# Optimization experiments

Measured on AMD Instinct MI355X. Metric: run time of the kernel, lower is better.

The kernel has to match this reference:

```python
import jax, jax.numpy as jnp
import numpy as np

HIDDEN = 2048
HEADS = 16
HEAD_DIM = HIDDEN // HEADS          # 128
HALF = HEAD_DIM // 2                # 64
LATENT = HIDDEN // 4                # 512 (compression_ratio=4)
ROPE_BASE = 10000.0


def _rope_cos_sin(seq_len):
    # LlamaRotaryEmbedding with dim=HALF
    inv_freq = 1.0 / (ROPE_BASE ** (jnp.arange(0, HALF, 2, dtype=jnp.float32) / HALF))
    t = jnp.arange(seq_len, dtype=jnp.float32)
    freqs = jnp.einsum('i,j->ij', t, inv_freq)          # [S, HALF/2]
    emb = jnp.concatenate([freqs, freqs], axis=-1)       # [S, HALF]
    cos = jnp.cos(emb)[None, :, None, :]                 # [1,S,1,HALF]
    sin = jnp.sin(emb)[None, :, None, :]
    return cos, sin


def _rotate_half(x):
    x1, x2 = jnp.split(x, 2, axis=-1)
    return jnp.concatenate([-x2, x1], axis=-1)


def _apply_rope(x, cos, sin):
    return x * cos + _rotate_half(x) * sin


def setup_inputs() -> dict:
    key = jax.random.key(0)
    ks = jax.random.split(key, 10)
    B, S = 2, 2048
    std = 0.02
    inp = {
        'x':        jax.random.normal(ks[0], (B, S, HIDDEN), jnp.float32),
        # weights stored as [in, out] (transposed torch Linear weight)
        'W_kv_d':   jax.random.normal(ks[1], (HIDDEN, LATENT), jnp.float32) * std,
        'W_q_d':    jax.random.normal(ks[2], (HIDDEN, LATENT), jnp.float32) * std,
        'W_k_u':    jax.random.normal(ks[3], (LATENT, HEADS * HALF), jnp.float32) * std,
        'W_q_u':    jax.random.normal(ks[4], (LATENT, HEADS * HALF), jnp.float32) * std,
        'W_v_u':    jax.random.normal(ks[5], (LATENT, HIDDEN), jnp.float32) * std,
        'W_rope_k': jax.random.normal(ks[6], (HIDDEN, HIDDEN // 2), jnp.float32) * std,
        'W_rope_q': jax.random.normal(ks[7], (LATENT, HIDDEN // 2), jnp.float32) * std,
        'W_o':      jax.random.normal(ks[8], (HIDDEN, HIDDEN), jnp.float32) * std,
    }
    return inp


def reference(x, W_kv_d, W_q_d, W_k_u, W_q_u, W_v_u, W_rope_k, W_rope_q, W_o):
    B, S, _ = x.shape
    kv_latent = x @ W_kv_d                      # [B,S,LATENT]
    q_latent = x @ W_q_d                        # [B,S,LATENT]

    k = (kv_latent @ W_k_u).reshape(B, S, HEADS, HALF)
    q = (q_latent @ W_q_u).reshape(B, S, HEADS, HALF)
    v = (kv_latent @ W_v_u).reshape(B, S, HEADS, HEAD_DIM)

    q_rope = (q_latent @ W_rope_q).reshape(B, S, HEADS, HALF)
    k_rope = (x @ W_rope_k).reshape(B, S, HEADS, HALF)

    cos, sin = _rope_cos_sin(S)
    k_rope = _apply_rope(k_rope, cos, sin)
    q_rope = _apply_rope(q_rope, cos, sin)

    q = jnp.concatenate([q, q_rope], axis=-1)   # [B,S,H,HEAD_DIM]
    k = jnp.concatenate([k, k_rope], axis=-1)

    scale = 1.0 / jnp.sqrt(jnp.float32(HEAD_DIM))
    scores = jnp.einsum('bqhd,bkhd->bhqk', q, k) * scale   # [B,H,S,S]
    causal = jnp.tril(jnp.ones((S, S), dtype=bool))
    scores = jnp.where(causal[None, None], scores, jnp.float32(-1e30))
    attn = jax.nn.softmax(scores, axis=-1)
    y = jnp.einsum('bhqk,bkhd->bqhd', attn, v).reshape(B, S, HIDDEN)
    return y @ W_o
```

## Files before the change

### kernel.cpp

```cpp
#include <hip/hip_runtime.h>
#include <hip/hip_bf16.h>

typedef __hip_bfloat16 bf16;
typedef __attribute__((ext_vector_type(8))) short short8;
typedef __attribute__((ext_vector_type(4))) float f32x4;

#define AS1 __attribute__((address_space(1)))
#define AS3 __attribute__((address_space(3)))

__device__ __forceinline__ void gload_lds16(const bf16* gp, bf16* lp) {
  __builtin_amdgcn_global_load_lds((const AS1 void*)gp, (AS3 void*)lp, 16, 0, 0);
}

__device__ __forceinline__ float fast_exp2(float x) {
#if __has_builtin(__builtin_amdgcn_exp2f)
  return __builtin_amdgcn_exp2f(x);
#else
  return exp2f(x);
#endif
}

__device__ __forceinline__ void store_c(bf16* C, size_t idx, float v) { C[idx] = __float2bfloat16(v); }
__device__ __forceinline__ void store_c(float* C, size_t idx, float v) { C[idx] = v; }

struct __align__(8) b16x4 { bf16 a, b, c, d; };

__global__ void cvt_f32_bf16(const float* __restrict__ in, bf16* __restrict__ out) {
  const int i = (blockIdx.x * 256 + threadIdx.x) * 4;
  const float4 v = *(const float4*)(in + i);
  out[i + 0] = __float2bfloat16(v.x);
  out[i + 1] = __float2bfloat16(v.y);
  out[i + 2] = __float2bfloat16(v.z);
  out[i + 3] = __float2bfloat16(v.w);
}

struct PrepArgs {
  const float* src[8];
  bf16* dst[8];
  int R[8], C[8], cum[8];
};

__global__ void prep_kernel(PrepArgs a) {
  __shared__ bf16 t[32][33];
  const int blk = blockIdx.x;
  int e = 0;
  while (e < 7 && blk >= a.cum[e]) ++e;
  const int lt = blk - (e ? a.cum[e - 1] : 0);
  const int R = a.R[e], C = a.C[e];
  const int tpr = C >> 5;
  const int bx = lt % tpr, by = lt / tpr;
  const float* in = a.src[e];
  bf16* out = a.dst[e];
  const int c0 = bx * 32, r0 = by * 32;
  const int tx = threadIdx.x, ty = threadIdx.y;
  for (int i = 0; i < 4; ++i)
    t[ty + 8 * i][tx] = __float2bfloat16(in[(size_t)(r0 + ty + 8 * i) * C + c0 + tx]);
  __syncthreads();
  for (int i = 0; i < 4; ++i)
    out[(size_t)(c0 + ty + 8 * i) * R + r0 + tx] = t[tx][ty + 8 * i];
}

template <typename CT, int MODE>
__global__ void gemm_bt(const bf16* __restrict__ A, int lda,
                        const bf16* __restrict__ Bt,
                        CT* __restrict__ C, bf16* __restrict__ C2, int ldc,
                        int K)
{
  __shared__ __align__(16) bf16 As[128 * 32];
  __shared__ __align__(16) bf16 Bs[128 * 32];
  const int tid  = threadIdx.x;
  const int wave = tid >> 6, lane = tid & 63;
  const int quad = lane >> 4, l16 = lane & 15;
  const int m0 = blockIdx.y * 128, n0 = blockIdx.x * 128;
  const int wm = (wave >> 1) * 64, wn = (wave & 1) * 64;

  f32x4 acc[4][4];
#pragma unroll
  for (int i = 0; i < 4; ++i)
#pragma unroll
    for (int j = 0; j < 4; ++j) acc[i][j] = (f32x4){0.f, 0.f, 0.f, 0.f};

  const int r1  = tid >> 2;
  const int ks1 = (tid & 3) * 8;

  for (int k0 = 0; k0 < K; k0 += 32) {
    gload_lds16(A  + (size_t)(m0 + r1)      * lda + k0 + ks1, &As[tid * 8]);
    gload_lds16(A  + (size_t)(m0 + r1 + 64) * lda + k0 + ks1, &As[(tid + 256) * 8]);
    gload_lds16(Bt + (size_t)(n0 + r1)      * K   + k0 + ks1, &Bs[tid * 8]);
    gload_lds16(Bt + (size_t)(n0 + r1 + 64) * K   + k0 + ks1, &Bs[(tid + 256) * 8]);
    __syncthreads();

    short8 af[4], bf_[4];
#pragma unroll
    for (int mt = 0; mt < 4; ++mt)
      af[mt] = *(const short8*)&As[(wm + mt * 16 + l16) * 32 + quad * 8];
#pragma unroll
    for (int nt = 0; nt < 4; ++nt)
      bf_[nt] = *(const short8*)&Bs[(wn + nt * 16 + l16) * 32 + quad * 8];
#pragma unroll
    for (int mt = 0; mt < 4; ++mt)
#pragma unroll
      for (int nt = 0; nt < 4; ++nt)
        acc[mt][nt] = __builtin_amdgcn_mfma_f32_16x16x32_bf16(af[mt], bf_[nt], acc[mt][nt], 0, 0, 0);
    __syncthreads();
  }

#pragma unroll
  for (int mt = 0; mt < 4; ++mt) {
    const int row = m0 + wm + mt * 16 + quad * 4;
#pragma unroll
    for (int nt = 0; nt < 4; ++nt) {
      const int cn = n0 + wn + nt * 16 + l16;
      const f32x4 v = acc[mt][nt];
      if (MODE == 0) {
#pragma unroll
        for (int r = 0; r < 4; ++r)
          store_c(C, (size_t)(row + r) * ldc + cn, v[r]);
      } else if (MODE == 4) {
        if (cn < 1024) {
#pragma unroll
          for (int r = 0; r < 4; ++r)
            store_c(C, (size_t)(row + r) * 1024 + cn, v[r]);
        } else {
          const int cn2 = cn - 1024;
          const int g = ((cn2 >> 6) << 7) + 64 + (cn2 & 63);
#pragma unroll
          for (int r = 0; r < 4; ++r)
            C2[(size_t)(row + r) * 2048 + g] = __float2bfloat16(v[r]);
        }
      }
    }
  }
}

__global__ void gemm_up_fused(const bf16* __restrict__ latcat,
                              const bf16* __restrict__ wtUP,
                              const bf16* __restrict__ wtQcat,
                              bf16* __restrict__ vT, bf16* __restrict__ kfull,
                              bf16* __restrict__ qfull)
{
  const bool is2 = (blockIdx.x >= 24);
  const bf16* A  = latcat + (is2 ? 512 : 0);
  const bf16* Bt = is2 ? wtQcat : wtUP;
  const int n0 = (is2 ? (int)blockIdx.x - 24 : (int)blockIdx.x) * 128;
  const int K = 512, lda = 1024;

  __shared__ __align__(16) bf16 As[128 * 32];
  __shared__ __align__(16) bf16 Bs[128 * 32];
  const int tid  = threadIdx.x;
  const int wave = tid >> 6, lane = tid & 63;
  const int quad = lane >> 4, l16 = lane & 15;
  const int m0 = blockIdx.y * 128;
  const int wm = (wave >> 1) * 64, wn = (wave & 1) * 64;

  f32x4 acc[4][4];
#pragma unroll
  for (int i = 0; i < 4; ++i)
#pragma unroll
    for (int j = 0; j < 4; ++j) acc[i][j] = (f32x4){0.f, 0.f, 0.f, 0.f};

  const int r1  = tid >> 2;
  const int ks1 = (tid & 3) * 8;

  for (int k0 = 0; k0 < K; k0 += 32) {
    gload_lds16(A  + (size_t)(m0 + r1)      * lda + k0 + ks1, &As[tid * 8]);
    gload_lds16(A  + (size_t)(m0 + r1 + 64) * lda + k0 + ks1, &As[(tid + 256) * 8]);
    gload_lds16(Bt + (size_t)(n0 + r1)      * K   + k0 + ks1, &Bs[tid * 8]);
    gload_lds16(Bt + (size_t)(n0 + r1 + 64) * K   + k0 + ks1, &Bs[(tid + 256) * 8]);
    __syncthreads();

    short8 af[4], bf_[4];
#pragma unroll
    for (int mt = 0; mt < 4; ++mt)
      af[mt] = *(const short8*)&As[(wm + mt * 16 + l16) * 32 + quad * 8];
#pragma unroll
    for (int nt = 0; nt < 4; ++nt)
      bf_[nt] = *(const short8*)&Bs[(wn + nt * 16 + l16) * 32 + quad * 8];
#pragma unroll
    for (int mt = 0; mt < 4; ++mt)
#pragma unroll
      for (int nt = 0; nt < 4; ++nt)
        acc[mt][nt] = __builtin_amdgcn_mfma_f32_16x16x32_bf16(af[mt], bf_[nt], acc[mt][nt], 0, 0, 0);
    __syncthreads();
  }

  if (is2) {
#pragma unroll
    for (int mt = 0; mt < 4; ++mt) {
      const int row = m0 + wm + mt * 16 + quad * 4;
#pragma unroll
      for (int nt = 0; nt < 4; ++nt) {
        const int cn = n0 + wn + nt * 16 + l16;
        const int g = (((cn >> 6) & 15) << 7) + ((cn >> 10) << 6) + (cn & 63);
        const f32x4 v = acc[mt][nt];
#pragma unroll
        for (int r = 0; r < 4; ++r)
          qfull[(size_t)(row + r) * 2048 + g] = __float2bfloat16(v[r]);
      }
    }
  } else {
#pragma unroll
    for (int mt = 0; mt < 4; ++mt) {
      const int row = m0 + wm + mt * 16 + quad * 4;
#pragma unroll
      for (int nt = 0; nt < 4; ++nt) {
        const int cn = n0 + wn + nt * 16 + l16;
        const f32x4 v = acc[mt][nt];
        if (cn < 1024) {
          const int g = ((cn >> 6) << 7) + (cn & 63);
#pragma unroll
          for (int r = 0; r < 4; ++r)
            kfull[(size_t)(row + r) * 2048 + g] = __float2bfloat16(v[r]);
        } else {
          const int cn2 = cn - 1024;
          const int bb = row >> 11, s0 = row & 2047;
          b16x4 pk;
          pk.a = __float2bfloat16(v[0]); pk.b = __float2bfloat16(v[1]);
          pk.c = __float2bfloat16(v[2]); pk.d = __float2bfloat16(v[3]);
          *(b16x4*)(vT + ((size_t)(bb * 2048 + cn2)) * 2048 + s0) = pk;
        }
      }
    }
  }
}

__global__ void rope_kernel(bf16* __restrict__ q, bf16* __restrict__ k)
{
  const int idx = blockIdx.x * 256 + threadIdx.x;
  const int i = idx & 31;
  const int h = (idx >> 5) & 15;
  const int s = (idx >> 9) & 2047;
  const int b = idx >> 20;
  const size_t off = ((size_t)(b * 2048 + s)) * 2048 + h * 128 + 64;
  const float inv = fast_exp2(-(float)i * 0.41524101186092029f);
  const float ang = (float)s * inv;
  const float cs = cosf(ang), sn = sinf(ang);
  {
    bf16* p = q + off;
    const float x1 = __bfloat162float(p[i]);
    const float x2 = __bfloat162float(p[i + 32]);
    p[i]      = __float2bfloat16(x1 * cs - x2 * sn);
    p[i + 32] = __float2bfloat16(x2 * cs + x1 * sn);
  }
  {
    bf16* p = k + off;
    const float x1 = __bfloat162float(p[i]);
    const float x2 = __bfloat162float(p[i + 32]);
    p[i]      = __float2bfloat16(x1 * cs - x2 * sn);
    p[i + 32] = __float2bfloat16(x2 * cs + x1 * sn);
  }
}

__global__ __launch_bounds__(256, 2) void attn7_kernel(
    const bf16* __restrict__ Q, const bf16* __restrict__ Kf,
    const bf16* __restrict__ VT, bf16* __restrict__ Y)
{
  __shared__ __align__(16) bf16 Ks[64 * 128];
  __shared__ __align__(16) bf16 VTs[128 * 64];
  __shared__ __align__(16) bf16 Ps[4 * 32 * 64];
  const int tid  = threadIdx.x;
  const int wave = tid >> 6, lane = tid & 63;
  const int quad = lane >> 4, l16 = lane & 15;
  const int bh = blockIdx.x;
  const int yy = blockIdx.y;
  const int aa = yy & 7;
  const int qt = (yy >> 3) ? (15 - aa) : aa;
  const size_t kqbase = ((size_t)(bh >> 4) * 2048) * 2048 + (bh & 15) * 128;
  const size_t vtbase = (size_t)bh * 128 * 2048;
  const float C2 = 0.08838834764831845f * 1.4426950408889634f;
  const float MNEG = -30.0f;

  short8 ones;
#pragma unroll
  for (int i = 0; i < 8; ++i) ones[i] = (short)0x3F80;

  const int krow = tid >> 4, kcol = (tid & 15) * 8;
  const int vrow = tid >> 3, vcol = (tid & 7) * 8;

  const int q0 = qt * 128;
  const int T = 2 * qt + 2;
  const int wq0 = q0 + wave * 32;
  const int psbase = wave * (32 * 64);

  short8 qf[2][4];
#pragma unroll
  for (int m = 0; m < 2; ++m) {
    const bf16* qp = Q + kqbase + (size_t)(wq0 + m * 16 + l16) * 2048 + quad * 8;
#pragma unroll
    for (int kc = 0; kc < 4; ++kc) qf[m][kc] = *(const short8*)(qp + kc * 32);
  }
  f32x4 o[2][8];
#pragma unroll
  for (int m = 0; m < 2; ++m)
#pragma unroll
    for (int i = 0; i < 8; ++i) o[m][i] = (f32x4){0, 0, 0, 0};
  f32x4 lacc[2];
  lacc[0] = (f32x4){0, 0, 0, 0};
  lacc[1] = (f32x4){0, 0, 0, 0};

  short8 kg[4], vg[4];
#pragma unroll
  for (int i = 0; i < 4; ++i)
    kg[i] = *(const short8*)(Kf + kqbase + (size_t)(krow + i * 16) * 2048 + kcol);
#pragma unroll
  for (int i = 0; i < 4; ++i)
    vg[i] = *(const short8*)(VT + vtbase + (size_t)(vrow + i * 32) * 2048 + vcol);

  for (int t = 0; t < T; ++t) {
    const int k0 = t * 64;
    __syncthreads();
#pragma unroll
    for (int i = 0; i < 4; ++i) {
      const int rw = krow + i * 16;
      *(short8*)&Ks[rw * 128 + (kcol ^ ((rw & 7) * 8))] = kg[i];
    }
#pragma unroll
    for (int i = 0; i < 4; ++i) {
      const int rw = vrow + i * 32;
      *(short8*)&VTs[rw * 64 + (vcol ^ ((rw & 7) * 8))] = vg[i];
    }
    __syncthreads();
    if (t + 1 < T) {
      const int kn = k0 + 64;
#pragma unroll
      for (int i = 0; i < 4; ++i)
        kg[i] = *(const short8*)(Kf + kqbase + (size_t)(kn + krow + i * 16) * 2048 + kcol);
#pragma unroll
      for (int i = 0; i < 4; ++i)
        vg[i] = *(const short8*)(VT + vtbase + (size_t)(vrow + i * 32) * 2048 + kn + vcol);
    }

    if (k0 <= wq0 + 31) {
      f32x4 sf[2][4];
#pragma unroll
      for (int m = 0; m < 2; ++m)
#pragma unroll
        for (int kt = 0; kt < 4; ++kt) sf[m][kt] = (f32x4){0, 0, 0, 0};
#pragma unroll
      for (int kt = 0; kt < 4; ++kt) {
#pragma unroll
        for (int kc = 0; kc < 4; ++kc) {
          const short8 bfr = *(const short8*)&Ks[(kt * 16 + l16) * 128 +
                                                ((kc * 32 + quad * 8) ^ ((l16 & 7) * 8))];
          sf[0][kt] = __builtin_amdgcn_mfma_f32_16x16x32_bf16(qf[0][kc], bfr, sf[0][kt], 0, 0, 0);
          sf[1][kt] = __builtin_amdgcn_mfma_f32_16x16x32_bf16(qf[1][kc], bfr, sf[1][kt], 0, 0, 0);
        }
      }
#pragma unroll
      for (int m = 0; m < 2; ++m) {
        const int row0m = wq0 + m * 16 + quad * 4;
        if (k0 + 63 > row0m) {
#pragma unroll
          for (int kt = 0; kt < 4; ++kt) {
            const int col = k0 + kt * 16 + l16;
#pragma unroll
            for (int r = 0; r < 4; ++r)
              sf[m][kt][r] = (col > row0m + r) ? -3e38f : sf[m][kt][r];
          }
        }
      }
#pragma unroll
      for (int m = 0; m < 2; ++m)
#pragma unroll
        for (int kt = 0; kt < 4; ++kt)
#pragma unroll
          for (int r = 0; r < 4; ++r) {
            const float p = fast_exp2(__builtin_fmaf(sf[m][kt][r], C2, MNEG));
            const int prow = m * 16 + quad * 4 + r;
            const int pcol = (kt * 16 + l16) ^ (quad * 16);
            Ps[psbase + prow * 64 + pcol] = __float2bfloat16(p);
          }
      asm volatile("s_waitcnt lgkmcnt(0)" ::: "memory");
#pragma unroll
      for (int kc = 0; kc < 2; ++kc) {
        short8 ap[2];
#pragma unroll
        for (int m = 0; m < 2; ++m) {
          const int acol = (kc * 32 + quad * 8) ^ (((l16 >> 2) & 3) * 16);
          ap[m] = *(const short8*)&Ps[psbase + (m * 16 + l16) * 64 + acol];
          lacc[m] = __builtin_amdgcn_mfma_f32_16x16x32_bf16(ap[m], ones, lacc[m], 0, 0, 0);
        }
#pragma unroll
        for (int dt = 0; dt < 8; ++dt) {
          const short8 vb = *(const short8*)&VTs[(dt * 16 + l16) * 64 +
                                                ((kc * 32 + quad * 8) ^ ((l16 & 7) * 8))];
          o[0][dt] = __builtin_amdgcn_mfma_f32_16x16x32_bf16(ap[0], vb, o[0][dt], 0, 0, 0);
          o[1][dt] = __builtin_amdgcn_mfma_f32_16x16x32_bf16(ap[1], vb, o[1][dt], 0, 0, 0);
        }
      }
    }
  }

#pragma unroll
  for (int m = 0; m < 2; ++m) {
    const int row0m = wq0 + m * 16 + quad * 4;
#pragma unroll
    for (int r = 0; r < 4; ++r) {
      const float inv = 1.0f / lacc[m][r];
#pragma unroll
      for (int dt = 0; dt < 8; ++dt)
        Y[kqbase + (size_t)(row0m + r) * 2048 + dt * 16 + l16] =
            __float2bfloat16(o[m][dt][r] * inv);
    }
  }
}

extern "C" void kernel_launch(void* const* d_in, const int* in_sizes, int n_in,
                              void* d_out, int out_size, void* d_ws, size_t ws_size,
                              hipStream_t stream)
{
  const float* x      = (const float*)d_in[0];
  const float* Wkvd   = (const float*)d_in[1];
  const float* Wqd    = (const float*)d_in[2];
  const float* Wku    = (const float*)d_in[3];
  const float* Wqu    = (const float*)d_in[4];
  const float* Wvu    = (const float*)d_in[5];
  const float* Wropek = (const float*)d_in[6];
  const float* Wropeq = (const float*)d_in[7];
  const float* Wo     = (const float*)d_in[8];

  char* ws = (char*)d_ws;
  size_t off = 0;
  auto alloc = [&](size_t elems) {
    bf16* p = (bf16*)(ws + off);
    off += ((elems * sizeof(bf16) + 255) & ~(size_t)255);
    return p;
  };
  bf16* wtX    = alloc((size_t)2048 * 2048);
  bf16* wtUP   = alloc((size_t)3072 * 512);
  bf16* wtQcat = alloc((size_t)2048 * 512);
  bf16* latcat = alloc((size_t)4096 * 1024);
  bf16* wt_o   = alloc((size_t)2048 * 2048);
  bf16* xbf    = alloc((size_t)4096 * 2048);
  bf16* qfull  = alloc((size_t)4096 * 2048);
  bf16* kfull  = alloc((size_t)4096 * 2048);
  bf16* ybuf   = (bf16*)ws;
  bf16* vT     = (bf16*)d_out;
  (void)ws_size; (void)in_sizes; (void)n_in; (void)out_size;

  cvt_f32_bf16<<<8192, 256, 0, stream>>>(x, xbf);

  PrepArgs pa;
  const float* srcs[8] = {Wkvd, Wqd, Wropek, Wku, Wvu, Wqu, Wropeq, Wo};
  bf16* dsts[8] = {wtX, wtX + (size_t)512 * 2048, wtX + (size_t)1024 * 2048,
                   wtUP, wtUP + (size_t)1024 * 512,
                   wtQcat, wtQcat + (size_t)1024 * 512, wt_o};
  const int Rs[8] = {2048, 2048, 2048, 512, 512, 512, 512, 2048};
  const int Cs[8] = {512, 512, 1024, 1024, 2048, 1024, 1024, 2048};
  int cum = 0;
  for (int e = 0; e < 8; ++e) {
    pa.src[e] = srcs[e]; pa.dst[e] = dsts[e]; pa.R[e] = Rs[e]; pa.C[e] = Cs[e];
    cum += (Rs[e] >> 5) * (Cs[e] >> 5);
    pa.cum[e] = cum;
  }
  prep_kernel<<<cum, dim3(32, 8), 0, stream>>>(pa);

  gemm_bt<bf16, 4><<<dim3(16, 32), 256, 0, stream>>>(xbf, 2048, wtX, latcat, kfull, 1024, 2048);
  gemm_up_fused<<<dim3(40, 32), 256, 0, stream>>>(latcat, wtUP, wtQcat, vT, kfull, qfull);

  rope_kernel<<<(2 * 2048 * 16 * 32) / 256, 256, 0, stream>>>(qfull, kfull);
  attn7_kernel<<<dim3(32, 16), 256, 0, stream>>>(qfull, kfull, vT, ybuf);
  gemm_bt<float, 0><<<dim3(16, 32), 256, 0, stream>>>(ybuf, 2048, wt_o, (float*)d_out, (bf16*)nullptr, 2048, 2048);
}
```

Baseline: 331.2 us.

## Pair low and high 64-row query blocks per workgroup for causal balance

Result: slower. 344.2 us (+3.9%).

```diff
diff --git a/kernel.cpp b/kernel.cpp
--- a/kernel.cpp
+++ b/kernel.cpp
@@ -251,7 +251,86 @@
   }
 }
 
-__global__ __launch_bounds__(256, 2) void attn7_kernel(
+template <bool LO>
+__device__ __forceinline__ void attn_tile(
+    const bf16* Ks, const bf16* VTs, bf16* Psw,
+    const short8 (&qf)[2][4], const short8& ones,
+    f32x4 (&o)[2][8], f32x4 (&lacc)[2],
+    int quad, int l16, int k0,
+    int row0_lo, int row0_hi, bool mask_lo, bool mask_hi,
+    float C2, float MNEG)
+{
+  f32x4 sf[2][4];
+#pragma unroll
+  for (int kt = 0; kt < 4; ++kt) {
+    sf[0][kt] = (f32x4){0, 0, 0, 0};
+    sf[1][kt] = (f32x4){0, 0, 0, 0};
+  }
+#pragma unroll
+  for (int kt = 0; kt < 4; ++kt) {
+#pragma unroll
+    for (int kc = 0; kc < 4; ++kc) {
+      const short8 bfr = *(const short8*)&Ks[(kt * 16 + l16) * 128 +
+                                            ((kc * 32 + quad * 8) ^ ((l16 & 7) * 8))];
+      sf[1][kt] = __builtin_amdgcn_mfma_f32_16x16x32_bf16(qf[1][kc], bfr, sf[1][kt], 0, 0, 0);
+      if (LO)
+        sf[0][kt] = __builtin_amdgcn_mfma_f32_16x16x32_bf16(qf[0][kc], bfr, sf[0][kt], 0, 0, 0);
+    }
+  }
+  if (LO && mask_lo) {
+#pragma unroll
+    for (int kt = 0; kt < 4; ++kt) {
+      const int col = k0 + kt * 16 + l16;
+#pragma unroll
+      for (int r = 0; r < 4; ++r)
+        sf[0][kt][r] = (col > row0_lo + r) ? -3e38f : sf[0][kt][r];
+    }
+  }
+  if (mask_hi) {
+#pragma unroll
+    for (int kt = 0; kt < 4; ++kt) {
+      const int col = k0 + kt * 16 + l16;
+#pragma unroll
+      for (int r = 0; r < 4; ++r)
+        sf[1][kt][r] = (col > row0_hi + r) ? -3e38f : sf[1][kt][r];
+    }
+  }
+#pragma unroll
+  for (int m = 0; m < 2; ++m) {
+    if (!LO && m == 0) continue;
+#pragma unroll
+    for (int kt = 0; kt < 4; ++kt)
+#pragma unroll
+      for (int r = 0; r < 4; ++r) {
+        const float p = fast_exp2(__builtin_fmaf(sf[m][kt][r], C2, MNEG));
+        const int prow = m * 16 + quad * 4 + r;
+        const int pcol = (kt * 16 + l16) ^ (quad * 16);
+        Psw[prow * 64 + pcol] = __float2bfloat16(p);
+      }
+  }
+  asm volatile("s_waitcnt lgkmcnt(0)" ::: "memory");
+#pragma unroll
+  for (int kc = 0; kc < 2; ++kc) {
+    short8 ap[2];
+    const int acol = (kc * 32 + quad * 8) ^ (((l16 >> 2) & 3) * 16);
+    if (LO) {
+      ap[0] = *(const short8*)&Psw[l16 * 64 + acol];
+      lacc[0] = __builtin_amdgcn_mfma_f32_16x16x32_bf16(ap[0], ones, lacc[0], 0, 0, 0);
+    }
+    ap[1] = *(const short8*)&Psw[(16 + l16) * 64 + acol];
+    lacc[1] = __builtin_amdgcn_mfma_f32_16x16x32_bf16(ap[1], ones, lacc[1], 0, 0, 0);
+#pragma unroll
+    for (int dt = 0; dt < 8; ++dt) {
+      const short8 vb = *(const short8*)&VTs[(dt * 16 + l16) * 64 +
+                                            ((kc * 32 + quad * 8) ^ ((l16 & 7) * 8))];
+      if (LO)
+        o[0][dt] = __builtin_amdgcn_mfma_f32_16x16x32_bf16(ap[0], vb, o[0][dt], 0, 0, 0);
+      o[1][dt] = __builtin_amdgcn_mfma_f32_16x16x32_bf16(ap[1], vb, o[1][dt], 0, 0, 0);
+    }
+  }
+}
+
+__global__ __launch_bounds__(256, 2) void attn8_kernel(
     const bf16* __restrict__ Q, const bf16* __restrict__ Kf,
     const bf16* __restrict__ VT, bf16* __restrict__ Y)
 {
@@ -264,7 +343,7 @@
   const int bh = blockIdx.x;
   const int yy = blockIdx.y;
   const int aa = yy & 7;
-  const int qt = (yy >> 3) ? (15 - aa) : aa;
+  const int a = (yy >> 3) ? (15 - aa) : aa;
   const size_t kqbase = ((size_t)(bh >> 4) * 2048) * 2048 + (bh & 15) * 128;
   const size_t vtbase = (size_t)bh * 128 * 2048;
   const float C2 = 0.08838834764831845f * 1.4426950408889634f;
@@ -277,17 +356,21 @@
   const int krow = tid >> 4, kcol = (tid & 15) * 8;
   const int vrow = tid >> 3, vcol = (tid & 7) * 8;
 
-  const int q0 = qt * 128;
-  const int T = 2 * qt + 2;
-  const int wq0 = q0 + wave * 32;
+  const int T = 32 - a;
+  const int lo0 = a * 64 + wave * 16;
+  const int hi0 = (31 - a) * 64 + wave * 16;
   const int psbase = wave * (32 * 64);
 
   short8 qf[2][4];
-#pragma unroll
-  for (int m = 0; m < 2; ++m) {
-    const bf16* qp = Q + kqbase + (size_t)(wq0 + m * 16 + l16) * 2048 + quad * 8;
-#pragma unroll
-    for (int kc = 0; kc < 4; ++kc) qf[m][kc] = *(const short8*)(qp + kc * 32);
+  {
+    const bf16* qp = Q + kqbase + (size_t)(lo0 + l16) * 2048 + quad * 8;
+#pragma unroll
+    for (int kc = 0; kc < 4; ++kc) qf[0][kc] = *(const short8*)(qp + kc * 32);
+  }
+  {
+    const bf16* qp = Q + kqbase + (size_t)(hi0 + l16) * 2048 + quad * 8;
+#pragma unroll
+    for (int kc = 0; kc < 4; ++kc) qf[1][kc] = *(const short8*)(qp + kc * 32);
   }
   f32x4 o[2][8];
 #pragma unroll
@@ -330,70 +413,19 @@
         vg[i] = *(const short8*)(VT + vtbase + (size_t)(vrow + i * 32) * 2048 + kn + vcol);
     }
 
-    if (k0 <= wq0 + 31) {
-      f32x4 sf[2][4];
-#pragma unroll
-      for (int m = 0; m < 2; ++m)
-#pragma unroll
-        for (int kt = 0; kt < 4; ++kt) sf[m][kt] = (f32x4){0, 0, 0, 0};
-#pragma unroll
-      for (int kt = 0; kt < 4; ++kt) {
-#pragma unroll
-        for (int kc = 0; kc < 4; ++kc) {
-          const short8 bfr = *(const short8*)&Ks[(kt * 16 + l16) * 128 +
-                                                ((kc * 32 + quad * 8) ^ ((l16 & 7) * 8))];
-          sf[0][kt] = __builtin_amdgcn_mfma_f32_16x16x32_bf16(qf[0][kc], bfr, sf[0][kt], 0, 0, 0);
-          sf[1][kt] = __builtin_amdgcn_mfma_f32_16x16x32_bf16(qf[1][kc], bfr, sf[1][kt], 0, 0, 0);
-        }
-      }
-#pragma unroll
-      for (int m = 0; m < 2; ++m) {
-        const int row0m = wq0 + m * 16 + quad * 4;
-        if (k0 + 63 > row0m) {
-#pragma unroll
-          for (int kt = 0; kt < 4; ++kt) {
-            const int col = k0 + kt * 16 + l16;
-#pragma unroll
-            for (int r = 0; r < 4; ++r)
-              sf[m][kt][r] = (col > row0m + r) ? -3e38f : sf[m][kt][r];
-          }
-        }
-      }
-#pragma unroll
-      for (int m = 0; m < 2; ++m)
-#pragma unroll
-        for (int kt = 0; kt < 4; ++kt)
-#pragma unroll
-          for (int r = 0; r < 4; ++r) {
-            const float p = fast_exp2(__builtin_fmaf(sf[m][kt][r], C2, MNEG));
-            const int prow = m * 16 + quad * 4 + r;
-            const int pcol = (kt * 16 + l16) ^ (quad * 16);
-            Ps[psbase + prow * 64 + pcol] = __float2bfloat16(p);
-          }
-      asm volatile("s_waitcnt lgkmcnt(0)" ::: "memory");
-#pragma unroll
-      for (int kc = 0; kc < 2; ++kc) {
-        short8 ap[2];
-#pragma unroll
-        for (int m = 0; m < 2; ++m) {
-          const int acol = (kc * 32 + quad * 8) ^ (((l16 >> 2) & 3) * 16);
-          ap[m] = *(const short8*)&Ps[psbase + (m * 16 + l16) * 64 + acol];
-          lacc[m] = __builtin_amdgcn_mfma_f32_16x16x32_bf16(ap[m], ones, lacc[m], 0, 0, 0);
-        }
-#pragma unroll
-        for (int dt = 0; dt < 8; ++dt) {
-          const short8 vb = *(const short8*)&VTs[(dt * 16 + l16) * 64 +
-                                                ((kc * 32 + quad * 8) ^ ((l16 & 7) * 8))];
-          o[0][dt] = __builtin_amdgcn_mfma_f32_16x16x32_bf16(ap[0], vb, o[0][dt], 0, 0, 0);
-          o[1][dt] = __builtin_amdgcn_mfma_f32_16x16x32_bf16(ap[1], vb, o[1][dt], 0, 0, 0);
-        }
-      }
-    }
+    const bool mask_lo = (t == a);
+    const bool mask_hi = (t == T - 1);
+    if (t <= a)
+      attn_tile<true>(Ks, VTs, Ps + psbase, qf, ones, o, lacc, quad, l16, k0,
+                      lo0 + quad * 4, hi0 + quad * 4, mask_lo, mask_hi, C2, MNEG);
+    else
+      attn_tile<false>(Ks, VTs, Ps + psbase, qf, ones, o, lacc, quad, l16, k0,
+                       lo0 + quad * 4, hi0 + quad * 4, mask_lo, mask_hi, C2, MNEG);
   }
 
 #pragma unroll
   for (int m = 0; m < 2; ++m) {
-    const int row0m = wq0 + m * 16 + quad * 4;
+    const int row0m = (m ? hi0 : lo0) + quad * 4;
 #pragma unroll
     for (int r = 0; r < 4; ++r) {
       const float inv = 1.0f / lacc[m][r];
@@ -459,6 +491,6 @@
   gemm_up_fused<<<dim3(40, 32), 256, 0, stream>>>(latcat, wtUP, wtQcat, vT, kfull, qfull);
 
   rope_kernel<<<(2 * 2048 * 16 * 32) / 256, 256, 0, stream>>>(qfull, kfull);
-  attn7_kernel<<<dim3(32, 16), 256, 0, stream>>>(qfull, kfull, vT, ybuf);
+  attn8_kernel<<<dim3(32, 16), 256, 0, stream>>>(qfull, kfull, vT, ybuf);
   gemm_bt<float, 0><<<dim3(16, 32), 256, 0, stream>>>(ybuf, 2048, wt_o, (float*)d_out, (bf16*)nullptr, 2048, 2048);
 }
```

## Balance causal attention work by splitting query tiles across paired blocks

Applied to the files above, without the earlier changes.

Result: slower. 405.9 us (+22.5%).

```diff
diff --git a/kernel.cpp b/kernel.cpp
--- a/kernel.cpp
+++ b/kernel.cpp
@@ -251,9 +251,127 @@
   }
 }
 
-__global__ __launch_bounds__(256, 2) void attn7_kernel(
+__device__ __forceinline__ void attn_phase(
     const bf16* __restrict__ Q, const bf16* __restrict__ Kf,
-    const bf16* __restrict__ VT, bf16* __restrict__ Y)
+    const bf16* __restrict__ VT,
+    size_t kqbase, size_t vtbase, int qt, int t0, int t1,
+    bf16* __restrict__ Ks, bf16* __restrict__ VTs, bf16* __restrict__ Psw,
+    f32x4 (&o)[2][8], f32x4 (&lacc)[2], const short8 ones,
+    int wave, int quad, int l16, int krow, int kcol, int vrow, int vcol)
+{
+  const float C2 = 0.08838834764831845f * 1.4426950408889634f;
+  const float MNEG = -30.0f;
+  const int wq0 = qt * 128 + wave * 32;
+
+  short8 qf[2][4];
+#pragma unroll
+  for (int m = 0; m < 2; ++m) {
+    const bf16* qp = Q + kqbase + (size_t)(wq0 + m * 16 + l16) * 2048 + quad * 8;
+#pragma unroll
+    for (int kc = 0; kc < 4; ++kc) qf[m][kc] = *(const short8*)(qp + kc * 32);
+  }
+
+  short8 kg[4], vg[4];
+  {
+    const int kk = t0 * 64;
+#pragma unroll
+    for (int i = 0; i < 4; ++i)
+      kg[i] = *(const short8*)(Kf + kqbase + (size_t)(kk + krow + i * 16) * 2048 + kcol);
+#pragma unroll
+    for (int i = 0; i < 4; ++i)
+      vg[i] = *(const short8*)(VT + vtbase + (size_t)(vrow + i * 32) * 2048 + kk + vcol);
+  }
+
+  for (int t = t0; t < t1; ++t) {
+    const int k0 = t * 64;
+    __syncthreads();
+#pragma unroll
+    for (int i = 0; i < 4; ++i) {
+      const int rw = krow + i * 16;
+      *(short8*)&Ks[rw * 128 + (kcol ^ ((rw & 7) * 8))] = kg[i];
+    }
+#pragma unroll
+    for (int i = 0; i < 4; ++i) {
+      const int rw = vrow + i * 32;
+      *(short8*)&VTs[rw * 64 + (vcol ^ ((rw & 7) * 8))] = vg[i];
+    }
+    __syncthreads();
+    if (t + 1 < t1) {
+      const int kn = k0 + 64;
+#pragma unroll
+      for (int i = 0; i < 4; ++i)
+        kg[i] = *(const short8*)(Kf + kqbase + (size_t)(kn + krow + i * 16) * 2048 + kcol);
+#pragma unroll
+      for (int i = 0; i < 4; ++i)
+        vg[i] = *(const short8*)(VT + vtbase + (size_t)(vrow + i * 32) * 2048 + kn + vcol);
+    }
+    if (k0 > wq0 + 31) continue;
+
+    f32x4 sf[2][4];
+#pragma unroll
+    for (int kt = 0; kt < 4; ++kt) {
+      sf[0][kt] = (f32x4){0, 0, 0, 0};
+      sf[1][kt] = (f32x4){0, 0, 0, 0};
+    }
+#pragma unroll
+    for (int kt = 0; kt < 4; ++kt) {
+#pragma unroll
+      for (int kc = 0; kc < 4; ++kc) {
+        const short8 bfr = *(const short8*)&Ks[(kt * 16 + l16) * 128 +
+                                              ((kc * 32 + quad * 8) ^ ((l16 & 7) * 8))];
+        sf[0][kt] = __builtin_amdgcn_mfma_f32_16x16x32_bf16(qf[0][kc], bfr, sf[0][kt], 0, 0, 0);
+        sf[1][kt] = __builtin_amdgcn_mfma_f32_16x16x32_bf16(qf[1][kc], bfr, sf[1][kt], 0, 0, 0);
+      }
+    }
+#pragma unroll
+    for (int m = 0; m < 2; ++m) {
+      const int row0m = wq0 + m * 16 + quad * 4;
+      if (k0 + 63 > row0m) {
+#pragma unroll
+        for (int kt = 0; kt < 4; ++kt) {
+          const int col = k0 + kt * 16 + l16;
+#pragma unroll
+          for (int r = 0; r < 4; ++r)
+            sf[m][kt][r] = (col > row0m + r) ? -3e38f : sf[m][kt][r];
+        }
+      }
+    }
+#pragma unroll
+    for (int m = 0; m < 2; ++m)
+#pragma unroll
+      for (int kt = 0; kt < 4; ++kt)
+#pragma unroll
+        for (int r = 0; r < 4; ++r) {
+          const float p = fast_exp2(__builtin_fmaf(sf[m][kt][r], C2, MNEG));
+          const int prow = m * 16 + quad * 4 + r;
+          const int pcol = (kt * 16 + l16) ^ (quad * 16);
+          Psw[prow * 64 + pcol] = __float2bfloat16(p);
+        }
+    asm volatile("s_waitcnt lgkmcnt(0)" ::: "memory");
+#pragma unroll
+    for (int kc = 0; kc < 2; ++kc) {
+      short8 ap[2];
+      const int acol = (kc * 32 + quad * 8) ^ (((l16 >> 2) & 3) * 16);
+      ap[0] = *(const short8*)&Psw[l16 * 64 + acol];
+      lacc[0] = __builtin_amdgcn_mfma_f32_16x16x32_bf16(ap[0], ones, lacc[0], 0, 0, 0);
+      ap[1] = *(const short8*)&Psw[(16 + l16) * 64 + acol];
+      lacc[1] = __builtin_amdgcn_mfma_f32_16x16x32_bf16(ap[1], ones, lacc[1], 0, 0, 0);
+#pragma unroll
+      for (int dt = 0; dt < 8; ++dt) {
+        const short8 vb = *(const short8*)&VTs[(dt * 16 + l16) * 64 +
+                                              ((kc * 32 + quad * 8) ^ ((l16 & 7) * 8))];
+        o[0][dt] = __builtin_amdgcn_mfma_f32_16x16x32_bf16(ap[0], vb, o[0][dt], 0, 0, 0);
+        o[1][dt] = __builtin_amdgcn_mfma_f32_16x16x32_bf16(ap[1], vb, o[1][dt], 0, 0, 0);
+      }
+    }
+  }
+}
+
+__global__ __launch_bounds__(256, 2) void attn9_kernel(
+    const bf16* __restrict__ Q, const bf16* __restrict__ Kf,
+    const bf16* __restrict__ VT, bf16* __restrict__ Y,
+    bf16* __restrict__ part_o, float* __restrict__ part_l,
+    unsigned* __restrict__ flags)
 {
   __shared__ __align__(16) bf16 Ks[64 * 128];
   __shared__ __align__(16) bf16 VTs[128 * 64];
@@ -262,13 +380,11 @@
   const int wave = tid >> 6, lane = tid & 63;
   const int quad = lane >> 4, l16 = lane & 15;
   const int bh = blockIdx.x;
-  const int yy = blockIdx.y;
-  const int aa = yy & 7;
-  const int qt = (yy >> 3) ? (15 - aa) : aa;
+  const int j  = blockIdx.y;
+  const int qt_b = 15 - j;
+  const int qt_a = j;
   const size_t kqbase = ((size_t)(bh >> 4) * 2048) * 2048 + (bh & 15) * 128;
   const size_t vtbase = (size_t)bh * 128 * 2048;
-  const float C2 = 0.08838834764831845f * 1.4426950408889634f;
-  const float MNEG = -30.0f;
 
   short8 ones;
 #pragma unroll
@@ -276,132 +392,68 @@
 
   const int krow = tid >> 4, kcol = (tid & 15) * 8;
   const int vrow = tid >> 3, vcol = (tid & 7) * 8;
-
-  const int q0 = qt * 128;
-  const int T = 2 * qt + 2;
-  const int wq0 = q0 + wave * 32;
-  const int psbase = wave * (32 * 64);
-
-  short8 qf[2][4];
-#pragma unroll
-  for (int m = 0; m < 2; ++m) {
-    const bf16* qp = Q + kqbase + (size_t)(wq0 + m * 16 + l16) * 2048 + quad * 8;
-#pragma unroll
-    for (int kc = 0; kc < 4; ++kc) qf[m][kc] = *(const short8*)(qp + kc * 32);
-  }
+  bf16* Psw = Ps + wave * (32 * 64);
+
   f32x4 o[2][8];
+  f32x4 lacc[2];
+
 #pragma unroll
   for (int m = 0; m < 2; ++m)
 #pragma unroll
     for (int i = 0; i < 8; ++i) o[m][i] = (f32x4){0, 0, 0, 0};
-  f32x4 lacc[2];
   lacc[0] = (f32x4){0, 0, 0, 0};
   lacc[1] = (f32x4){0, 0, 0, 0};
-
-  short8 kg[4], vg[4];
-#pragma unroll
-  for (int i = 0; i < 4; ++i)
-    kg[i] = *(const short8*)(Kf + kqbase + (size_t)(krow + i * 16) * 2048 + kcol);
-#pragma unroll
-  for (int i = 0; i < 4; ++i)
-    vg[i] = *(const short8*)(VT + vtbase + (size_t)(vrow + i * 32) * 2048 + vcol);
-
-  for (int t = 0; t < T; ++t) {
-    const int k0 = t * 64;
-    __syncthreads();
-#pragma unroll
-    for (int i = 0; i < 4; ++i) {
-      const int rw = krow + i * 16;
-      *(short8*)&Ks[rw * 128 + (kcol ^ ((rw & 7) * 8))] = kg[i];
-    }
-#pragma unroll
-    for (int i = 0; i < 4; ++i) {
-      const int rw = vrow + i * 32;
-      *(short8*)&VTs[rw * 64 + (vcol ^ ((rw & 7) * 8))] = vg[i];
-    }
-    __syncthreads();
-    if (t + 1 < T) {
-      const int kn = k0 + 64;
-#pragma unroll
-      for (int i = 0; i < 4; ++i)
-        kg[i] = *(const short8*)(Kf + kqbase + (size_t)(kn + krow + i * 16) * 2048 + kcol);
-#pragma unroll
-      for (int i = 0; i < 4; ++i)
-        vg[i] = *(const short8*)(VT + vtbase + (size_t)(vrow + i * 32) * 2048 + kn + vcol);
-    }
-
-    if (k0 <= wq0 + 31) {
-      f32x4 sf[2][4];
-#pragma unroll
-      for (int m = 0; m < 2; ++m)
-#pragma unroll
-        for (int kt = 0; kt < 4; ++kt) sf[m][kt] = (f32x4){0, 0, 0, 0};
-#pragma unroll
-      for (int kt = 0; kt < 4; ++kt) {
-#pragma unroll
-        for (int kc = 0; kc < 4; ++kc) {
-          const short8 bfr = *(const short8*)&Ks[(kt * 16 + l16) * 128 +
-                                                ((kc * 32 + quad * 8) ^ ((l16 & 7) * 8))];
-          sf[0][kt] = __builtin_amdgcn_mfma_f32_16x16x32_bf16(qf[0][kc], bfr, sf[0][kt], 0, 0, 0);
-          sf[1][kt] = __builtin_amdgcn_mfma_f32_16x16x32_bf16(qf[1][kc], bfr, sf[1][kt], 0, 0, 0);
+  attn_phase(Q, Kf, VT, kqbase, vtbase, qt_b, qt_b + 1, 2 * qt_b + 2,
+             Ks, VTs, Psw, o, lacc, ones, wave, quad, l16, krow, kcol, vrow, vcol);
+  {
+    bf16* po = part_o + ((size_t)(bh * 16 + qt_b) << 14);
+    float* pl = part_l + ((bh * 16 + qt_b) << 7);
+#pragma unroll
+    for (int m = 0; m < 2; ++m)
+#pragma unroll
+      for (int r = 0; r < 4; ++r) {
+        const int rl = wave * 32 + m * 16 + quad * 4 + r;
+#pragma unroll
+        for (int dt = 0; dt < 8; ++dt)
+          po[rl * 128 + dt * 16 + l16] = __float2bfloat16(o[m][dt][r]);
+        if (l16 == 0) pl[rl] = lacc[m][r];
+      }
+    __threadfence();
+    __syncthreads();
+    if (tid == 0)
+      __hip_atomic_store(&flags[bh * 16 + qt_b], 1u, __ATOMIC_RELEASE,
+                         __HIP_MEMORY_SCOPE_AGENT);
+  }
+
+#pragma unroll
+  for (int m = 0; m < 2; ++m)
+#pragma unroll
+    for (int i = 0; i < 8; ++i) o[m][i] = (f32x4){0, 0, 0, 0};
+  lacc[0] = (f32x4){0, 0, 0, 0};
+  lacc[1] = (f32x4){0, 0, 0, 0};
+  attn_phase(Q, Kf, VT, kqbase, vtbase, qt_a, 0, qt_a + 1,
+             Ks, VTs, Psw, o, lacc, ones, wave, quad, l16, krow, kcol, vrow, vcol);
+
+  {
+    const unsigned* fl = &flags[bh * 16 + qt_a];
+    while (__hip_atomic_load(fl, __ATOMIC_ACQUIRE, __HIP_MEMORY_SCOPE_AGENT) == 0u)
+      __builtin_amdgcn_s_sleep(2);
+    const bf16* po = part_o + ((size_t)(bh * 16 + qt_a) << 14);
+    const float* pl = part_l + ((bh * 16 + qt_a) << 7);
+#pragma unroll
+    for (int m = 0; m < 2; ++m)
+#pragma unroll
+      for (int r = 0; r < 4; ++r) {
+        const int rl = wave * 32 + m * 16 + quad * 4 + r;
+        const float lt = lacc[m][r] + pl[rl];
+        const float inv = 1.0f / lt;
+#pragma unroll
+        for (int dt = 0; dt < 8; ++dt) {
+          const float y = o[m][dt][r] + __bfloat162float(po[rl * 128 + dt * 16 + l16]);
+          Y[kqbase + (size_t)(qt_a * 128 + rl) * 2048 + dt * 16 + l16] =
+              __float2bfloat16(y * inv);
         }
       }
-#pragma unroll
-      for (int m = 0; m < 2; ++m) {
-        const int row0m = wq0 + m * 16 + quad * 4;
-        if (k0 + 63 > row0m) {
-#pragma unroll
-          for (int kt = 0; kt < 4; ++kt) {
-            const int col = k0 + kt * 16 + l16;
-#pragma unroll
-            for (int r = 0; r < 4; ++r)
-              sf[m][kt][r] = (col > row0m + r) ? -3e38f : sf[m][kt][r];
-          }
-        }
-      }
-#pragma unroll
-      for (int m = 0; m < 2; ++m)
-#pragma unroll
-        for (int kt = 0; kt < 4; ++kt)
-#pragma unroll
-          for (int r = 0; r < 4; ++r) {
-            const float p = fast_exp2(__builtin_fmaf(sf[m][kt][r], C2, MNEG));
-            const int prow = m * 16 + quad * 4 + r;
-            const int pcol = (kt * 16 + l16) ^ (quad * 16);
-            Ps[psbase + prow * 64 + pcol] = __float2bfloat16(p);
-          }
-      asm volatile("s_waitcnt lgkmcnt(0)" ::: "memory");
-#pragma unroll
-      for (int kc = 0; kc < 2; ++kc) {
-        short8 ap[2];
-#pragma unroll
-        for (int m = 0; m < 2; ++m) {
-          const int acol = (kc * 32 + quad * 8) ^ (((l16 >> 2) & 3) * 16);
-          ap[m] = *(const short8*)&Ps[psbase + (m * 16 + l16) * 64 + acol];
-          lacc[m] = __builtin_amdgcn_mfma_f32_16x16x32_bf16(ap[m], ones, lacc[m], 0, 0, 0);
-        }
-#pragma unroll
-        for (int dt = 0; dt < 8; ++dt) {
-          const short8 vb = *(const short8*)&VTs[(dt * 16 + l16) * 64 +
-                                                ((kc * 32 + quad * 8) ^ ((l16 & 7) * 8))];
-          o[0][dt] = __builtin_amdgcn_mfma_f32_16x16x32_bf16(ap[0], vb, o[0][dt], 0, 0, 0);
-          o[1][dt] = __builtin_amdgcn_mfma_f32_16x16x32_bf16(ap[1], vb, o[1][dt], 0, 0, 0);
-        }
-      }
-    }
-  }
-
-#pragma unroll
-  for (int m = 0; m < 2; ++m) {
-    const int row0m = wq0 + m * 16 + quad * 4;
-#pragma unroll
-    for (int r = 0; r < 4; ++r) {
-      const float inv = 1.0f / lacc[m][r];
-#pragma unroll
-      for (int dt = 0; dt < 8; ++dt)
-        Y[kqbase + (size_t)(row0m + r) * 2048 + dt * 16 + l16] =
-            __float2bfloat16(o[m][dt][r] * inv);
-    }
   }
 }
 
@@ -436,6 +488,9 @@
   bf16* kfull  = alloc((size_t)4096 * 2048);
   bf16* ybuf   = (bf16*)ws;
   bf16* vT     = (bf16*)d_out;
+  bf16*     part_o = xbf;
+  float*    part_l = (float*)(ws + 16777216);
+  unsigned* flags  = (unsigned*)(ws + 16777216 + 262144);
   (void)ws_size; (void)in_sizes; (void)n_in; (void)out_size;
 
   cvt_f32_bf16<<<8192, 256, 0, stream>>>(x, xbf);
@@ -459,6 +514,9 @@
   gemm_up_fused<<<dim3(40, 32), 256, 0, stream>>>(latcat, wtUP, wtQcat, vT, kfull, qfull);
 
   rope_kernel<<<(2 * 2048 * 16 * 32) / 256, 256, 0, stream>>>(qfull, kfull);
-  attn7_kernel<<<dim3(32, 16), 256, 0, stream>>>(qfull, kfull, vT, ybuf);
+
+  hipMemsetAsync(flags, 0, 32 * 16 * sizeof(unsigned), stream);
+  attn9_kernel<<<dim3(32, 16), 256, 0, stream>>>(qfull, kfull, vT, ybuf,
+                                                 part_o, part_l, flags);
   gemm_bt<float, 0><<<dim3(16, 32), 256, 0, stream>>>(ybuf, 2048, wt_o, (float*)d_out, (bf16*)nullptr, 2048, 2048);
 }
```
